# Kernel tuning notes

Measured on AMD Instinct MI355X. Metric: run time of the kernel, lower is better.

Reference implementation:

```python
import jax, jax.numpy as jnp
import numpy as np

EPS = 1e-6
BN_EPS = 1e-5


def point_cells(loc_orig, H, W):
    # map [-1,1] xy coords to nearest cell index on an HxW grid
    loc = jnp.clip(loc_orig, -1.0, 1.0) * 0.5 + 0.5
    cx = jnp.clip(jnp.round(loc[..., 0] * (W - 1)), 0, W - 1).astype(jnp.int32)
    cy = jnp.clip(jnp.round(loc[..., 1] * (H - 1)), 0, H - 1).astype(jnp.int32)
    return cx + cy * W  # (B, N0)


def token2map(x, loc_orig, idx_agg, H, W):
    # scatter token features to an HxW map, averaging per cell
    B, N, C = x.shape
    N0 = loc_orig.shape[1]
    cell = point_cells(loc_orig, H, W)                      # (B, N0)
    feat = jnp.take_along_axis(x, idx_agg[..., None], axis=1)  # (B, N0, C)
    flat = (cell + jnp.arange(B)[:, None] * (H * W)).reshape(-1)
    s = jax.ops.segment_sum(feat.reshape(-1, C), flat, num_segments=B * H * W)
    cnt = jax.ops.segment_sum(jnp.ones((B * N0,), x.dtype), flat, num_segments=B * H * W)
    x_map = s / (cnt[:, None] + EPS)
    return x_map.reshape(B, H, W, C)


def map2token(x_map, N, loc_orig, idx_agg, agg_weight):
    # gather map features at original point locations, aggregate per token
    B, H, W, C = x_map.shape
    cell = point_cells(loc_orig, H, W)
    feat = jnp.take_along_axis(x_map.reshape(B, H * W, C), cell[..., None], axis=1)  # (B, N0, C)
    v = agg_weight.reshape(B, -1, 1)
    tflat = (idx_agg + jnp.arange(B)[:, None] * N).reshape(-1)
    s = jax.ops.segment_sum((feat * v).reshape(-1, C), tflat, num_segments=B * N)
    norm = jax.ops.segment_sum(v.reshape(-1), tflat, num_segments=B * N)
    return (s / (norm[:, None] + EPS)).reshape(B, N, C)


def token_cluster_grid(x, loc_orig, idx_agg, weight, H, W):
    # merge tokens into an (H//2)x(W//2) grid with confidence-weighted averaging
    B, N, C = x.shape
    H2, W2 = H // 2, W // 2
    Ns = H2 * W2
    cell = point_cells(loc_orig, H2, W2)                           # (B, N0) new token per point
    v = jnp.take_along_axis(weight, idx_agg[..., None], axis=1)     # (B, N0, 1)
    feat = jnp.take_along_axis(x, idx_agg[..., None], axis=1)       # (B, N0, C)
    flat = (cell + jnp.arange(B)[:, None] * Ns).reshape(-1)
    s = jax.ops.segment_sum((feat * v).reshape(-1, C), flat, num_segments=B * Ns)
    norm = jax.ops.segment_sum(v.reshape(-1), flat, num_segments=B * Ns) + EPS
    x_down = (s / norm[:, None]).reshape(B, Ns, C)
    weight_t = (v.reshape(-1) / norm[flat]).reshape(B, -1, 1)       # per-point normalized weight
    return x_down, cell, weight_t


def reference(x, loc_orig, idx_agg, agg_weight, conv_w, conv_b, skip_w, bn_gamma, bn_beta, conf_w, conf_b, H, W):
    B, N, C = x.shape
    x_map = token2map(x, loc_orig, idx_agg, H, W)  # (B, H, W, C)
    y = jax.lax.conv_general_dilated(
        x_map, conv_w, window_strides=(2, 2), padding=((1, 1), (1, 1)),
        dimension_numbers=('NHWC', 'HWIO', 'NHWC')) + conv_b  # (B, H/2, W/2, dim_out)
    xt = map2token(y, N, loc_orig, idx_agg, agg_weight) + x @ skip_w  # (B, N, dim_out)
    # BatchNorm over (B, N) per channel (training-mode batch stats)
    mean = jnp.mean(xt, axis=(0, 1))
    var = jnp.var(xt, axis=(0, 1))
    xt = (xt - mean) * jax.lax.rsqrt(var + BN_EPS) * bn_gamma + bn_beta
    conf = xt @ conf_w + conf_b          # (B, N, 1)
    weight = jnp.exp(conf)
    x_down, idx_agg_down, weight_t = token_cluster_grid(xt, loc_orig, idx_agg, weight, H, W)
    agg_weight_down = agg_weight * weight_t
    agg_weight_down = agg_weight_down / jnp.max(agg_weight_down, axis=1, keepdims=True)
    x_down = jax.nn.relu(x_down)
    x_act = jax.nn.relu(xt)
    return x_down, idx_agg_down, agg_weight_down, x_act, conf


def setup_inputs() -> dict:
    key = jax.random.key(0)
    ks = jax.random.split(key, 8)
    B, N, C, Cout, H, W = 64, 4096, 64, 128, 64, 64
    x = jax.random.normal(ks[0], (B, N, C), dtype=jnp.float32)
    loc_orig = jax.random.uniform(ks[1], (B, N, 2), dtype=jnp.float32, minval=-1.0, maxval=1.0)
    idx_agg = jax.random.randint(ks[2], (B, N), 0, N, dtype=jnp.int32)
    agg_weight = jax.random.uniform(ks[3], (B, N, 1), dtype=jnp.float32, minval=0.1, maxval=1.0)
    conv_w = jax.random.normal(ks[4], (3, 3, C, Cout), dtype=jnp.float32) * (1.0 / np.sqrt(9 * C))
    conv_b = jnp.zeros((Cout,), jnp.float32)
    skip_w = jax.random.normal(ks[5], (C, Cout), dtype=jnp.float32) * (1.0 / np.sqrt(C))
    bn_gamma = jnp.ones((Cout,), jnp.float32)
    bn_beta = jnp.zeros((Cout,), jnp.float32)
    conf_w = jax.random.normal(ks[6], (Cout, 1), dtype=jnp.float32) * (1.0 / np.sqrt(Cout))
    conf_b = jnp.zeros((1,), jnp.float32)
    return {"x": x, "loc_orig": loc_orig, "idx_agg": idx_agg, "agg_weight": agg_weight,
            "conv_w": conv_w, "conv_b": conv_b, "skip_w": skip_w,
            "bn_gamma": bn_gamma, "bn_beta": bn_beta, "conf_w": conf_w, "conf_b": conf_b,
            "H": H, "W": W}
```

## Files before the change

### kernel.cpp

```cpp
#include <hip/hip_runtime.h>

#define BB 64
#define NN 4096
#define CCH 64
#define CO 128
#define HH 64
#define WW 64
#define H2 32
#define W2 32
#define EPSF 1e-6f
#define BNEPS 1e-5f

typedef unsigned short ushort_t;
using bf8  = __attribute__((ext_vector_type(8))) short;
using f32x4 = __attribute__((ext_vector_type(4))) float;

__device__ inline ushort_t f2bf(float f) {
  unsigned u = __float_as_uint(f);
  unsigned r = (u + 0x7fffu + ((u >> 16) & 1u)) >> 16;
  return (ushort_t)r;
}
__device__ inline float bflo(unsigned u) { return __uint_as_float(u << 16); }
__device__ inline float bfhi(unsigned u) { return __uint_as_float(u & 0xffff0000u); }

__device__ inline void gload_lds16(const void* src, void* ldsdst) {
  __builtin_amdgcn_global_load_lds((const __attribute__((address_space(1))) void*)src,
                                   (__attribute__((address_space(3))) void*)ldsdst, 16, 0, 0);
}

__device__ inline void cells_from_loc(float lx, float ly, int& c64, int& c32) {
  lx = fminf(fmaxf(lx, -1.f), 1.f) * 0.5f + 0.5f;
  ly = fminf(fmaxf(ly, -1.f), 1.f) * 0.5f + 0.5f;
  int cx = (int)fminf(fmaxf(rintf(lx * (WW - 1)), 0.f), (float)(WW - 1));
  int cy = (int)fminf(fmaxf(rintf(ly * (HH - 1)), 0.f), (float)(HH - 1));
  c64 = cx + cy * WW;
  int cx2 = (int)fminf(fmaxf(rintf(lx * (W2 - 1)), 0.f), (float)(W2 - 1));
  int cy2 = (int)fminf(fmaxf(rintf(ly * (H2 - 1)), 0.f), (float)(H2 - 1));
  c32 = cx2 + cy2 * W2;
}

__global__ __launch_bounds__(256) void k_prep(const float* __restrict__ loc, const int* __restrict__ idxagg,
                                              const float* __restrict__ aw,
                                              float* __restrict__ idx_out,
                                              unsigned* __restrict__ pck64, unsigned* __restrict__ pck32,
                                              unsigned* __restrict__ pckT, float* __restrict__ nrm) {
  int i = blockIdx.x * 256 + threadIdx.x;
  int b = i >> 12;
  int c64, c2;
  cells_from_loc(loc[2 * i], loc[2 * i + 1], c64, c2);
  idx_out[i] = (float)c2;
  atomicAdd(&pck64[(b << 12) + c64], 1u);
  atomicAdd(&pck32[(b << 10) + c2], 1u);
  atomicAdd(&pckT[(b << 12) + idxagg[i]], 1u);
  unsafeAtomicAdd(&nrm[(b << 12) + idxagg[i]], aw[i]);
}

__global__ __launch_bounds__(256) void k_wprep(const float* __restrict__ convw, const float* __restrict__ skipw,
                                               ushort_t* __restrict__ wT, ushort_t* __restrict__ swT) {
  int e = blockIdx.x * 256 + threadIdx.x;
  if (e < 9 * CCH * CO) {
    int co = e & 127, k = e >> 7;
    wT[co * 576 + k] = f2bf(convw[k * CO + co]);
  } else {
    int e2 = e - 9 * CCH * CO;
    int co = e2 & 127, k = e2 >> 7;
    swT[co * 64 + k] = f2bf(skipw[k * CO + co]);
  }
}

__device__ void block_exscan_pack(unsigned* __restrict__ buf, int L) {
  __shared__ int partial[256];
  int tid = threadIdx.x;
  int per = L >> 8;
  int base = tid * per;
  int s = 0;
  for (int i = 0; i < per; i++) s += (int)buf[base + i];
  __syncthreads();
  partial[tid] = s;
  __syncthreads();
  for (int d = 1; d < 256; d <<= 1) {
    int v = (tid >= d) ? partial[tid - d] : 0;
    __syncthreads();
    partial[tid] += v;
    __syncthreads();
  }
  int run = (tid == 0) ? 0 : partial[tid - 1];
  for (int i = 0; i < per; i++) {
    int n = (int)buf[base + i];
    buf[base + i] = ((unsigned)run << 16) | (unsigned)run;
    run += n;
  }
}

__global__ __launch_bounds__(256) void k_scan(unsigned* __restrict__ pck64, unsigned* __restrict__ pckT,
                                              unsigned* __restrict__ pck32) {
  int b = blockIdx.x;
  block_exscan_pack(pck64 + ((size_t)b << 12), 4096);
  block_exscan_pack(pckT + ((size_t)b << 12), 4096);
  block_exscan_pack(pck32 + ((size_t)b << 10), 1024);
}

__global__ __launch_bounds__(256) void k_fill(const float* __restrict__ loc, const int* __restrict__ idxagg,
                                              const float* __restrict__ aw,
                                              unsigned* __restrict__ pck64, unsigned* __restrict__ pckT,
                                              unsigned* __restrict__ pck32,
                                              ushort_t* __restrict__ list64, unsigned* __restrict__ listT,
                                              ushort_t* __restrict__ list32) {
  int i = blockIdx.x * 256 + threadIdx.x;
  int b = i >> 12;
  int c64, c2;
  cells_from_loc(loc[2 * i], loc[2 * i + 1], c64, c2);
  int idx = idxagg[i];
  unsigned pos = atomicAdd(&pck64[(b << 12) + c64], 1u) & 0xffffu;
  list64[(b << 12) + pos] = (ushort_t)idx;
  pos = atomicAdd(&pckT[(b << 12) + idx], 1u) & 0xffffu;
  listT[(b << 12) + pos] = ((unsigned)c2 << 16) | (unsigned)f2bf(aw[i]);
  pos = atomicAdd(&pck32[(b << 10) + c2], 1u) & 0xffffu;
  list32[(b << 12) + pos] = (ushort_t)idx;
}

__global__ __launch_bounds__(256) void k_border(ushort_t* __restrict__ xmb) {
  int t = blockIdx.x * 256 + threadIdx.x;
  int q = t & 15;
  int cell = (t >> 4) % 260;
  int b = t / (260 * 16);
  int r, c;
  if (cell < 66)       { r = 0;  c = cell; }
  else if (cell < 132) { r = 65; c = cell - 66; }
  else if (cell < 196) { r = cell - 132 + 1; c = 0; }
  else                 { r = cell - 196 + 1; c = 65; }
  *(uint2*)&xmb[(((size_t)(b * 66 + r)) * 66 + c) * 64 + q * 4] = make_uint2(0u, 0u);
}

__global__ __launch_bounds__(256) void k_t2m(const float* __restrict__ x,
                                             const unsigned* __restrict__ pck64,
                                             const ushort_t* __restrict__ list64, ushort_t* __restrict__ xmb) {
  int blk = blockIdx.x;
  int sblk = (blk & 7) * 8192 + (blk >> 3);
  int g = sblk * 4 + (threadIdx.x >> 6);
  int lane = threadIdx.x & 63;
  int b = g >> 12, cell = g & 4095;
  unsigned v = pck64[g];
  int o = (int)(v >> 16), n = (int)(v & 0xffffu) - o;
  const ushort_t* lp = list64 + ((size_t)b << 12) + o;
  const float* xb = x + ((size_t)b << 18);
  float s0 = 0.f, s1 = 0.f, s2 = 0.f, s3 = 0.f;
  int i = 0;
  for (; i + 4 <= n; i += 4) {
    int i0 = lp[i], i1 = lp[i + 1], i2 = lp[i + 2], i3 = lp[i + 3];
    s0 += xb[(size_t)i0 * 64 + lane];
    s1 += xb[(size_t)i1 * 64 + lane];
    s2 += xb[(size_t)i2 * 64 + lane];
    s3 += xb[(size_t)i3 * 64 + lane];
  }
  for (; i < n; i++) s0 += xb[(size_t)lp[i] * 64 + lane];
  float avg = (s0 + s1 + s2 + s3) / ((float)n + EPSF);
  int r = cell >> 6, cc = cell & 63;
  xmb[(((size_t)(b * 66 + r + 1)) * 66 + cc + 1) * 64 + lane] = f2bf(avg);
}

__global__ __launch_bounds__(256) void k_conv(const ushort_t* __restrict__ xmb, const ushort_t* __restrict__ wT,
                                              const float* __restrict__ cb, float* __restrict__ y) {
  __shared__ ushort_t A[2][4096];
  const int tid = threadIdx.x;
  const int wave = tid >> 6, lane = tid & 63;
  const int m0 = blockIdx.x * 128;

  f32x4 acc[2][8];
  {
    float bv[8];
#pragma unroll
    for (int nt = 0; nt < 8; nt++) bv[nt] = cb[nt * 16 + (lane & 15)];
#pragma unroll
    for (int mt = 0; mt < 2; mt++)
#pragma unroll
      for (int nt = 0; nt < 8; nt++) {
        f32x4 a; a[0] = bv[nt]; a[1] = bv[nt]; a[2] = bv[nt]; a[3] = bv[nt];
        acc[mt][nt] = a;
      }
  }

  const int srcslot = (((lane & 3) ^ ((lane >> 3) & 3))) * 8;
  int sb[2], soy[2], sox[2];
#pragma unroll
  for (int q = 0; q < 2; q++) {
    int r = wave * 32 + q * 16 + (lane >> 2);
    int s = m0 + r;
    sb[q] = s >> 10; soy[q] = (s >> 5) & 31; sox[q] = s & 31;
  }

  auto stage = [&](int ks, int buf) {
    int kp = ks >> 1, ci0 = (ks & 1) * 32;
    int ky = kp / 3, kx = kp - ky * 3;
#pragma unroll
    for (int q = 0; q < 2; q++) {
      int iy = 2 * soy[q] + ky, ix = 2 * sox[q] + kx;
      const ushort_t* src = xmb + (((size_t)sb[q] * 66 + iy) * 66 + ix) * 64 + ci0 + srcslot;
      gload_lds16(src, &A[buf][(wave * 32 + q * 16) * 32]);
    }
  };

  stage(0, 0);
  const int rdslotx = (lane >> 1) & 3;
  for (int ks = 0; ks < 18; ks++) {
    int buf = ks & 1;
    __syncthreads();
    if (ks < 17) stage(ks + 1, buf ^ 1);
    bf8 a[2];
#pragma unroll
    for (int mt = 0; mt < 2; mt++) {
      int r = wave * 32 + mt * 16 + (lane & 15);
      int slot = (lane >> 4) ^ rdslotx;
      a[mt] = *(const bf8*)&A[buf][r * 32 + slot * 8];
    }
    int k0 = ks * 32 + (lane >> 4) * 8;
#pragma unroll
    for (int nt = 0; nt < 8; nt++) {
      int co = nt * 16 + (lane & 15);
      bf8 bbf = *(const bf8*)&wT[co * 576 + k0];
      acc[0][nt] = __builtin_amdgcn_mfma_f32_16x16x32_bf16(a[0], bbf, acc[0][nt], 0, 0, 0);
      acc[1][nt] = __builtin_amdgcn_mfma_f32_16x16x32_bf16(a[1], bbf, acc[1][nt], 0, 0, 0);
    }
  }
#pragma unroll
  for (int mt = 0; mt < 2; mt++)
#pragma unroll
    for (int nt = 0; nt < 8; nt++) {
      int co = nt * 16 + (lane & 15);
#pragma unroll
      for (int j = 0; j < 4; j++) {
        int srow = m0 + wave * 32 + mt * 16 + (lane >> 4) * 4 + j;
        y[(size_t)srow * 128 + co] = acc[mt][nt][j];
      }
    }
}

__global__ __launch_bounds__(256) void k_xt(const float* __restrict__ x, const ushort_t* __restrict__ swT,
                                            const float* __restrict__ y,
                                            const unsigned* __restrict__ listT, const unsigned* __restrict__ pckT,
                                            const float* __restrict__ nrm,
                                            ushort_t* __restrict__ XTB, float* __restrict__ BNP) {
  __shared__ float xg[64 * 128];
  __shared__ float nrminv[64];
  __shared__ float bnred[256];
  const int tid = threadIdx.x, wave = tid >> 6, lane = tid & 63;
  int blk = blockIdx.x;
  int sblk = (blk & 7) * 512 + (blk >> 3);
  const int t0 = sblk * 64;
  const int b = t0 >> 12, lt0 = t0 & 4095;

#pragma unroll
  for (int q = 0; q < 4; q++) {
    int ch = wave * 4 + q;
    int r = ch * 4 + (lane >> 4);
    int sp = lane & 15;
    const float* src = x + ((size_t)(t0 + r)) * 64 + ((sp ^ (r & 7)) << 2);
    gload_lds16(src, (char*)xg + ch * 1024);
  }
  if (tid < 64) nrminv[tid] = 1.f / (nrm[(b << 12) + lt0 + tid] + EPSF);
  bnred[tid] = 0.f;
  __syncthreads();

  bf8 afr[2];
  {
    int r = wave * 16 + (lane & 15);
#pragma unroll
    for (int ks = 0; ks < 2; ks++) {
      int cs = ks * 4 + (lane >> 4);
      const float4 f0 = *(const float4*)&xg[r * 64 + (((2 * cs) ^ (r & 7)) << 2)];
      const float4 f1 = *(const float4*)&xg[r * 64 + (((2 * cs + 1) ^ (r & 7)) << 2)];
      bf8 v;
      v[0] = (short)f2bf(f0.x); v[1] = (short)f2bf(f0.y);
      v[2] = (short)f2bf(f0.z); v[3] = (short)f2bf(f0.w);
      v[4] = (short)f2bf(f1.x); v[5] = (short)f2bf(f1.y);
      v[6] = (short)f2bf(f1.z); v[7] = (short)f2bf(f1.w);
      afr[ks] = v;
    }
  }

  f32x4 acc[8];
#pragma unroll
  for (int nt = 0; nt < 8; nt++) { f32x4 z; z[0] = 0; z[1] = 0; z[2] = 0; z[3] = 0; acc[nt] = z; }
#pragma unroll
  for (int ks = 0; ks < 2; ks++)
#pragma unroll
    for (int nt = 0; nt < 8; nt++) {
      int co = nt * 16 + (lane & 15);
      bf8 bbf = *(const bf8*)&swT[co * 64 + ks * 32 + (lane >> 4) * 8];
      acc[nt] = __builtin_amdgcn_mfma_f32_16x16x32_bf16(afr[ks], bbf, acc[nt], 0, 0, 0);
    }

  __syncthreads();

#pragma unroll
  for (int rr = 0; rr < 16; rr++) {
    *(float2*)&xg[(wave * 16 + rr) * 128 + ((2 * lane) ^ ((rr & 7) << 4))] = make_float2(0.f, 0.f);
  }

  {
    int gtok = lt0 + wave * 16 + lane;
    int myoff = 0;
    if (lane <= 16) myoff = (gtok >= NN) ? NN : (int)(pckT[(b << 12) + gtok] >> 16);
    int pbeg = __shfl(myoff, 0, 64), pend = __shfl(myoff, 16, 64);
    const unsigned* ltb = listT + ((size_t)b << 12);
    const float* yb = y + ((size_t)b << 17);
    for (int chunk = pbeg; chunk < pend; chunk += 64) {
      int pid = chunk + lane;
      unsigned rec = 0u;
      if (pid < pend) rec = ltb[pid];
      int rr = 0;
#pragma unroll
      for (int j = 1; j <= 16; j++) rr += (pid >= __shfl(myoff, j, 64)) ? 1 : 0;
      int nrec = min(64, pend - chunk);
      int i = 0;
      for (; i + 4 <= nrec; i += 4) {
        float2 yv[4]; float vv[4]; int rw[4];
#pragma unroll
        for (int u = 0; u < 4; u++) {
          unsigned rb = (unsigned)__shfl((int)rec, i + u, 64);
          vv[u] = __uint_as_float(rb << 16);
          rw[u] = __shfl(rr, i + u, 64);
          yv[u] = *(const float2*)&yb[(size_t)(rb >> 16) * 128 + lane * 2];
        }
#pragma unroll
        for (int u = 0; u < 4; u++) {
          float2* p = (float2*)&xg[(wave * 16 + rw[u]) * 128 + ((2 * lane) ^ ((rw[u] & 7) << 4))];
          float2 cv = *p;
          cv.x += yv[u].x * vv[u]; cv.y += yv[u].y * vv[u];
          *p = cv;
        }
      }
      for (; i < nrec; i++) {
        unsigned rb = (unsigned)__shfl((int)rec, i, 64);
        float v = __uint_as_float(rb << 16);
        int rw0 = __shfl(rr, i, 64);
        float2 yv0 = *(const float2*)&yb[(size_t)(rb >> 16) * 128 + lane * 2];
        float2* p = (float2*)&xg[(wave * 16 + rw0) * 128 + ((2 * lane) ^ ((rw0 & 7) << 4))];
        float2 cv = *p;
        cv.x += yv0.x * v; cv.y += yv0.y * v;
        *p = cv;
      }
    }
  }

#pragma unroll
  for (int nt = 0; nt < 8; nt++) {
    int co = nt * 16 + (lane & 15);
    float s = 0.f, q = 0.f;
#pragma unroll
    for (int j = 0; j < 4; j++) {
      int r = wave * 16 + (lane >> 4) * 4 + j;
      float val = acc[nt][j] + xg[r * 128 + (co ^ ((r & 7) << 4))] * nrminv[r];
      acc[nt][j] = val;
      s += val; q += val * val;
    }
    s += __shfl_xor(s, 16, 64); s += __shfl_xor(s, 32, 64);
    q += __shfl_xor(q, 16, 64); q += __shfl_xor(q, 32, 64);
    if (lane < 16) {
      atomicAdd(&bnred[nt * 16 + lane], s);
      atomicAdd(&bnred[128 + nt * 16 + lane], q);
    }
  }
  __syncthreads();

  ushort_t* xto = (ushort_t*)xg;
#pragma unroll
  for (int nt = 0; nt < 8; nt++) {
    int co = nt * 16 + (lane & 15);
#pragma unroll
    for (int j = 0; j < 4; j++) {
      int r = wave * 16 + (lane >> 4) * 4 + j;
      xto[r * 128 + (co ^ ((r & 7) << 4))] = f2bf(acc[nt][j]);
    }
  }
  __syncthreads();
#pragma unroll
  for (int it = 0; it < 4; it++) {
    int q8 = (it * 256 + tid) * 8;
    int r = q8 >> 7, c = q8 & 127;
    uint4 vv = *(const uint4*)&xto[r * 128 + (c ^ ((r & 7) << 4))];
    *(uint4*)&XTB[((size_t)t0) * 128 + q8] = vv;
  }
  unsafeAtomicAdd(&BNP[(blk & 63) * 256 + tid], bnred[tid]);
}

__global__ void k_bnfin(const float* __restrict__ BNP, const float* __restrict__ gamma,
                        const float* __restrict__ beta, float* __restrict__ ss) {
  int c = threadIdx.x;
  float s = 0.f, q = 0.f;
#pragma unroll 4
  for (int k = 0; k < 64; k++) {
    s += BNP[k * 256 + c];
    q += BNP[k * 256 + 128 + c];
  }
  float n = (float)(BB * NN);
  float mean = s / n;
  float var = q / n - mean * mean;
  float sc = gamma[c] * rsqrtf(var + BNEPS);
  ss[c] = sc;
  ss[128 + c] = beta[c] - mean * sc;
}

__global__ __launch_bounds__(256) void k_conf(const ushort_t* __restrict__ XTB, const float* __restrict__ ss,
                                              const float* __restrict__ confw, const float* __restrict__ confb,
                                              float* __restrict__ conf_out, float* __restrict__ wgt,
                                              float* __restrict__ xa) {
  int gid = blockIdx.x * 256 + threadIdx.x;
  int p = gid >> 6, lane = gid & 63;
  unsigned pw = *(const unsigned*)&XTB[(size_t)p * 128 + 2 * lane];
  const float2 sc = *(const float2*)&ss[2 * lane];
  const float2 sh = *(const float2*)&ss[128 + 2 * lane];
  float v0 = bflo(pw) * sc.x + sh.x;
  float v1 = bfhi(pw) * sc.y + sh.y;
  float2 xo; xo.x = fmaxf(v0, 0.f); xo.y = fmaxf(v1, 0.f);
  *(float2*)&xa[(size_t)p * 128 + 2 * lane] = xo;
  const float2 cw = *(const float2*)&confw[2 * lane];
  float s = v0 * cw.x + v1 * cw.y;
#pragma unroll
  for (int off = 32; off; off >>= 1) s += __shfl_down(s, off, 64);
  if (lane == 0) {
    float cf = s + confb[0];
    conf_out[p] = cf;
    wgt[p] = __expf(cf);
  }
}

__global__ __launch_bounds__(256) void k_cluster(const ushort_t* __restrict__ XTB, const float* __restrict__ ss,
                                                 const float* __restrict__ wgt,
                                                 const unsigned* __restrict__ pck32,
                                                 const ushort_t* __restrict__ list32,
                                                 float* __restrict__ xd, float* __restrict__ cnrm) {
  int blk = blockIdx.x;
  int sblk = (blk & 7) * 2048 + (blk >> 3);
  int wid = sblk * 4 + (threadIdx.x >> 6);
  int lane = threadIdx.x & 63;
  int b = wid >> 10;
  unsigned v = pck32[wid];
  int o = (int)(v >> 16), n = (int)(v & 0xffffu) - o;
  const ushort_t* lp = list32 + ((size_t)b << 12) + o;
  const float* wb = wgt + ((size_t)b << 12);
  const ushort_t* xtb = XTB + (((size_t)b) << 19);
  const float2 sc = *(const float2*)&ss[2 * lane];
  const float2 sh = *(const float2*)&ss[128 + 2 * lane];
  float s0 = 0.f, s1 = 0.f, sv = 0.f;
  int i = 0;
  for (; i + 2 <= n; i += 2) {
    int i0 = lp[i], i1 = lp[i + 1];
    float v0 = wb[i0], v1 = wb[i1];
    unsigned p0 = *(const unsigned*)&xtb[(size_t)i0 * 128 + 2 * lane];
    unsigned p1 = *(const unsigned*)&xtb[(size_t)i1 * 128 + 2 * lane];
    s0 += (bflo(p0) * sc.x + sh.x) * v0 + (bflo(p1) * sc.x + sh.x) * v1;
    s1 += (bfhi(p0) * sc.y + sh.y) * v0 + (bfhi(p1) * sc.y + sh.y) * v1;
    sv += v0 + v1;
  }
  if (i < n) {
    int i0 = lp[i];
    float v0 = wb[i0];
    unsigned p0 = *(const unsigned*)&xtb[(size_t)i0 * 128 + 2 * lane];
    s0 += (bflo(p0) * sc.x + sh.x) * v0;
    s1 += (bfhi(p0) * sc.y + sh.y) * v0;
    sv += v0;
  }
  float inv = 1.f / (sv + EPSF);
  float2 o2; o2.x = fmaxf(s0 * inv, 0.f); o2.y = fmaxf(s1 * inv, 0.f);
  *(float2*)&xd[(size_t)wid * 128 + 2 * lane] = o2;
  if (lane == 0) cnrm[wid] = sv;
}

__global__ __launch_bounds__(256) void k_awd(const float* __restrict__ loc, const float* __restrict__ wgt,
                                             const float* __restrict__ aw, const int* __restrict__ idxagg,
                                             const float* __restrict__ cnrm,
                                             float* __restrict__ awd, int* __restrict__ maxb) {
  int p = blockIdx.x * 256 + threadIdx.x;
  int b = p >> 12;
  int c64, c2;
  cells_from_loc(loc[2 * p], loc[2 * p + 1], c64, c2);
  float v = wgt[(b << 12) + idxagg[p]];
  float wt = v / (cnrm[(b << 10) + c2] + EPSF);
  float a = aw[p] * wt;
  awd[p] = a;
  float m = a;
#pragma unroll
  for (int off = 32; off; off >>= 1) m = fmaxf(m, __shfl_down(m, off, 64));
  if ((threadIdx.x & 63) == 0) atomicMax(&maxb[b], __float_as_int(m));
}

__global__ __launch_bounds__(256) void k_awdnorm(float* __restrict__ awd, const int* __restrict__ maxb) {
  int p = blockIdx.x * 256 + threadIdx.x;
  int b = p >> 12;
  awd[p] = awd[p] / __int_as_float(maxb[b]);
}

extern "C" void kernel_launch(void* const* d_in, const int* in_sizes, int n_in,
                              void* d_out, int out_size, void* d_ws, size_t ws_size,
                              hipStream_t stream) {
  (void)in_sizes; (void)n_in; (void)out_size;
  const float* x      = (const float*)d_in[0];
  const float* loc    = (const float*)d_in[1];
  const int*   idxagg = (const int*)  d_in[2];
  const float* aw     = (const float*)d_in[3];
  const float* convw  = (const float*)d_in[4];
  const float* convb  = (const float*)d_in[5];
  const float* skipw  = (const float*)d_in[6];
  const float* gamma  = (const float*)d_in[7];
  const float* beta   = (const float*)d_in[8];
  const float* confw  = (const float*)d_in[9];
  const float* confb  = (const float*)d_in[10];

  char* ws = (char*)d_ws;
  ushort_t* XTB   = (ushort_t*)(ws + 0);
  float*    Y     = (float*)  (ws + 67108864);
  ushort_t* XMB   = (ushort_t*)(ws + 100663296);
  float*    WGT   = (float*)  (ws + 100663296);
  float*    CNRM  = (float*)  (ws + 101711872);
  float*    BNP   = (float*)  (ws + 101974016);
  float*    SS    = (float*)  (ws + 102039552);
  int*      MAXB  = (int*)    (ws + 102040576);
  ushort_t* WT    = (ushort_t*)(ws + 136347648);
  ushort_t* SWT   = (ushort_t*)(ws + 136495104);
  float*    NRM   = (float*)  (ws + 136511488);
  unsigned* PCK64 = (unsigned*)(ws + 137560064);
  ushort_t* LIST64= (ushort_t*)(ws + 138608640);
  unsigned* PCKT  = (unsigned*)(ws + 139132928);
  unsigned* LISTT = (unsigned*)(ws + 140181504);
  unsigned* PCK32 = (unsigned*)(ws + 141230080);
  ushort_t* LIST32= (ushort_t*)(ws + 141492224);
  if (ws_size < 142016512) return;

  float* out    = (float*)d_out;
  float* O_XD   = out;
  float* O_IDX  = out + 8388608;
  float* O_AWD  = out + 8650752;
  float* XA     = out + 8912896;
  float* O_CONF = out + 42467328;

  hipMemsetAsync(PCK64, 0, 1048576, stream);
  hipMemsetAsync(PCKT, 0, 1048576, stream);
  hipMemsetAsync(PCK32, 0, 262144, stream);
  hipMemsetAsync(NRM, 0, 1048576, stream);

  k_prep   <<<1024,  256, 0, stream>>>(loc, idxagg, aw, O_IDX, PCK64, PCK32, PCKT, NRM);
  k_wprep  <<<320,   256, 0, stream>>>(convw, skipw, WT, SWT);
  k_scan   <<<64,    256, 0, stream>>>(PCK64, PCKT, PCK32);
  k_fill   <<<1024,  256, 0, stream>>>(loc, idxagg, aw, PCK64, PCKT, PCK32, LIST64, LISTT, LIST32);
  k_border <<<1040,  256, 0, stream>>>(XMB);
  k_t2m    <<<65536, 256, 0, stream>>>(x, PCK64, LIST64, XMB);
  k_conv   <<<512,   256, 0, stream>>>(XMB, WT, convb, Y);
  hipMemsetAsync(BNP, 0, 65536, stream);
  hipMemsetAsync(MAXB, 0, 256, stream);
  k_xt     <<<4096,  256, 0, stream>>>(x, SWT, Y, LISTT, PCKT, NRM, XTB, BNP);
  k_bnfin  <<<1,     128, 0, stream>>>(BNP, gamma, beta, SS);
  k_conf   <<<65536, 256, 0, stream>>>(XTB, SS, confw, confb, O_CONF, WGT, XA);
  k_cluster<<<16384, 256, 0, stream>>>(XTB, SS, WGT, PCK32, LIST32, O_XD, CNRM);
  k_awd    <<<1024,  256, 0, stream>>>(loc, WGT, aw, idxagg, CNRM, O_AWD, MAXB);
  k_awdnorm<<<1024,  256, 0, stream>>>(O_AWD, MAXB);
}
```

Measured before the change: 389.2 us.

## Fuse awd into cluster kernel, store conv output as bf16, consolidate memsets

Several changes land together. The conv output Y is stored as bf16 instead of fp32, which halves its write and gather traffic in k_xt at some precision cost. The k_awd kernel is folded into k_cluster: list32 now carries the point index, so the weights and the per-batch max are computed there. k_conf is vectorized to four channels per thread, k_scan is split across three times as many blocks, and the workspace is repacked so one memset covers all the zeroed buffers.

```diff
diff --git a/kernel.cpp b/kernel.cpp
--- a/kernel.cpp
+++ b/kernel.cpp
@@ -94,10 +94,10 @@
 
 __global__ __launch_bounds__(256) void k_scan(unsigned* __restrict__ pck64, unsigned* __restrict__ pckT,
                                               unsigned* __restrict__ pck32) {
-  int b = blockIdx.x;
-  block_exscan_pack(pck64 + ((size_t)b << 12), 4096);
-  block_exscan_pack(pckT + ((size_t)b << 12), 4096);
-  block_exscan_pack(pck32 + ((size_t)b << 10), 1024);
+  int b = blockIdx.x / 3, kind = blockIdx.x - 3 * (blockIdx.x / 3);
+  if (kind == 0)      block_exscan_pack(pck64 + ((size_t)b << 12), 4096);
+  else if (kind == 1) block_exscan_pack(pckT + ((size_t)b << 12), 4096);
+  else                block_exscan_pack(pck32 + ((size_t)b << 10), 1024);
 }
 
 __global__ __launch_bounds__(256) void k_fill(const float* __restrict__ loc, const int* __restrict__ idxagg,
@@ -105,9 +105,9 @@
                                               unsigned* __restrict__ pck64, unsigned* __restrict__ pckT,
                                               unsigned* __restrict__ pck32,
                                               ushort_t* __restrict__ list64, unsigned* __restrict__ listT,
-                                              ushort_t* __restrict__ list32) {
+                                              unsigned* __restrict__ list32) {
   int i = blockIdx.x * 256 + threadIdx.x;
-  int b = i >> 12;
+  int b = i >> 12, p = i & 4095;
   int c64, c2;
   cells_from_loc(loc[2 * i], loc[2 * i + 1], c64, c2);
   int idx = idxagg[i];
@@ -116,7 +116,7 @@
   pos = atomicAdd(&pckT[(b << 12) + idx], 1u) & 0xffffu;
   listT[(b << 12) + pos] = ((unsigned)c2 << 16) | (unsigned)f2bf(aw[i]);
   pos = atomicAdd(&pck32[(b << 10) + c2], 1u) & 0xffffu;
-  list32[(b << 12) + pos] = (ushort_t)idx;
+  list32[(b << 12) + pos] = ((unsigned)idx << 16) | (unsigned)p;
 }
 
 __global__ __launch_bounds__(256) void k_border(ushort_t* __restrict__ xmb) {
@@ -160,7 +160,7 @@
 }
 
 __global__ __launch_bounds__(256) void k_conv(const ushort_t* __restrict__ xmb, const ushort_t* __restrict__ wT,
-                                              const float* __restrict__ cb, float* __restrict__ y) {
+                                              const float* __restrict__ cb, ushort_t* __restrict__ y) {
   __shared__ ushort_t A[2][4096];
   const int tid = threadIdx.x;
   const int wave = tid >> 6, lane = tid & 63;
@@ -230,13 +230,13 @@
 #pragma unroll
       for (int j = 0; j < 4; j++) {
         int srow = m0 + wave * 32 + mt * 16 + (lane >> 4) * 4 + j;
-        y[(size_t)srow * 128 + co] = acc[mt][nt][j];
+        y[(size_t)srow * 128 + co] = f2bf(acc[mt][nt][j]);
       }
     }
 }
 
 __global__ __launch_bounds__(256) void k_xt(const float* __restrict__ x, const ushort_t* __restrict__ swT,
-                                            const float* __restrict__ y,
+                                            const ushort_t* __restrict__ y,
                                             const unsigned* __restrict__ listT, const unsigned* __restrict__ pckT,
                                             const float* __restrict__ nrm,
                                             ushort_t* __restrict__ XTB, float* __restrict__ BNP) {
@@ -303,7 +303,7 @@
     if (lane <= 16) myoff = (gtok >= NN) ? NN : (int)(pckT[(b << 12) + gtok] >> 16);
     int pbeg = __shfl(myoff, 0, 64), pend = __shfl(myoff, 16, 64);
     const unsigned* ltb = listT + ((size_t)b << 12);
-    const float* yb = y + ((size_t)b << 17);
+    const ushort_t* yb = y + ((size_t)b << 17);
     for (int chunk = pbeg; chunk < pend; chunk += 64) {
       int pid = chunk + lane;
       unsigned rec = 0u;
@@ -314,19 +314,19 @@
       int nrec = min(64, pend - chunk);
       int i = 0;
       for (; i + 4 <= nrec; i += 4) {
-        float2 yv[4]; float vv[4]; int rw[4];
+        unsigned yu[4]; float vv[4]; int rw[4];
 #pragma unroll
         for (int u = 0; u < 4; u++) {
           unsigned rb = (unsigned)__shfl((int)rec, i + u, 64);
           vv[u] = __uint_as_float(rb << 16);
           rw[u] = __shfl(rr, i + u, 64);
-          yv[u] = *(const float2*)&yb[(size_t)(rb >> 16) * 128 + lane * 2];
+          yu[u] = *(const unsigned*)&yb[(size_t)(rb >> 16) * 128 + lane * 2];
         }
 #pragma unroll
         for (int u = 0; u < 4; u++) {
           float2* p = (float2*)&xg[(wave * 16 + rw[u]) * 128 + ((2 * lane) ^ ((rw[u] & 7) << 4))];
           float2 cv = *p;
-          cv.x += yv[u].x * vv[u]; cv.y += yv[u].y * vv[u];
+          cv.x += bflo(yu[u]) * vv[u]; cv.y += bfhi(yu[u]) * vv[u];
           *p = cv;
         }
       }
@@ -334,10 +334,10 @@
         unsigned rb = (unsigned)__shfl((int)rec, i, 64);
         float v = __uint_as_float(rb << 16);
         int rw0 = __shfl(rr, i, 64);
-        float2 yv0 = *(const float2*)&yb[(size_t)(rb >> 16) * 128 + lane * 2];
+        unsigned yu0 = *(const unsigned*)&yb[(size_t)(rb >> 16) * 128 + lane * 2];
         float2* p = (float2*)&xg[(wave * 16 + rw0) * 128 + ((2 * lane) ^ ((rw0 & 7) << 4))];
         float2 cv = *p;
-        cv.x += yv0.x * v; cv.y += yv0.y * v;
+        cv.x += bflo(yu0) * v; cv.y += bfhi(yu0) * v;
         *p = cv;
       }
     }
@@ -406,19 +406,24 @@
                                               float* __restrict__ conf_out, float* __restrict__ wgt,
                                               float* __restrict__ xa) {
   int gid = blockIdx.x * 256 + threadIdx.x;
-  int p = gid >> 6, lane = gid & 63;
-  unsigned pw = *(const unsigned*)&XTB[(size_t)p * 128 + 2 * lane];
-  const float2 sc = *(const float2*)&ss[2 * lane];
-  const float2 sh = *(const float2*)&ss[128 + 2 * lane];
-  float v0 = bflo(pw) * sc.x + sh.x;
-  float v1 = bfhi(pw) * sc.y + sh.y;
-  float2 xo; xo.x = fmaxf(v0, 0.f); xo.y = fmaxf(v1, 0.f);
-  *(float2*)&xa[(size_t)p * 128 + 2 * lane] = xo;
-  const float2 cw = *(const float2*)&confw[2 * lane];
-  float s = v0 * cw.x + v1 * cw.y;
-#pragma unroll
-  for (int off = 32; off; off >>= 1) s += __shfl_down(s, off, 64);
-  if (lane == 0) {
+  int p = gid >> 5, l32 = gid & 31;
+  int c0 = l32 * 4;
+  const uint2 pw = *(const uint2*)&XTB[(size_t)p * 128 + c0];
+  const float4 sc = *(const float4*)&ss[c0];
+  const float4 sh = *(const float4*)&ss[128 + c0];
+  float v0 = bflo(pw.x) * sc.x + sh.x;
+  float v1 = bfhi(pw.x) * sc.y + sh.y;
+  float v2 = bflo(pw.y) * sc.z + sh.z;
+  float v3 = bfhi(pw.y) * sc.w + sh.w;
+  float4 xo;
+  xo.x = fmaxf(v0, 0.f); xo.y = fmaxf(v1, 0.f);
+  xo.z = fmaxf(v2, 0.f); xo.w = fmaxf(v3, 0.f);
+  *(float4*)&xa[(size_t)p * 128 + c0] = xo;
+  const float4 cw = *(const float4*)&confw[c0];
+  float s = v0 * cw.x + v1 * cw.y + v2 * cw.z + v3 * cw.w;
+#pragma unroll
+  for (int off = 16; off; off >>= 1) s += __shfl_down(s, off, 32);
+  if (l32 == 0) {
     float cf = s + confb[0];
     conf_out[p] = cf;
     wgt[p] = __expf(cf);
@@ -426,26 +431,30 @@
 }
 
 __global__ __launch_bounds__(256) void k_cluster(const ushort_t* __restrict__ XTB, const float* __restrict__ ss,
-                                                 const float* __restrict__ wgt,
+                                                 const float* __restrict__ wgt, const float* __restrict__ aw,
                                                  const unsigned* __restrict__ pck32,
-                                                 const ushort_t* __restrict__ list32,
-                                                 float* __restrict__ xd, float* __restrict__ cnrm) {
+                                                 const unsigned* __restrict__ list32,
+                                                 float* __restrict__ xd, float* __restrict__ awd,
+                                                 int* __restrict__ maxb) {
+  __shared__ float smax[4];
   int blk = blockIdx.x;
   int sblk = (blk & 7) * 2048 + (blk >> 3);
-  int wid = sblk * 4 + (threadIdx.x >> 6);
-  int lane = threadIdx.x & 63;
+  int wave = threadIdx.x >> 6, lane = threadIdx.x & 63;
+  int wid = sblk * 4 + wave;
   int b = wid >> 10;
   unsigned v = pck32[wid];
   int o = (int)(v >> 16), n = (int)(v & 0xffffu) - o;
-  const ushort_t* lp = list32 + ((size_t)b << 12) + o;
+  const unsigned* lp = list32 + ((size_t)b << 12) + o;
   const float* wb = wgt + ((size_t)b << 12);
+  const float* awb = aw + ((size_t)b << 12);
   const ushort_t* xtb = XTB + (((size_t)b) << 19);
   const float2 sc = *(const float2*)&ss[2 * lane];
   const float2 sh = *(const float2*)&ss[128 + 2 * lane];
   float s0 = 0.f, s1 = 0.f, sv = 0.f;
   int i = 0;
   for (; i + 2 <= n; i += 2) {
-    int i0 = lp[i], i1 = lp[i + 1];
+    unsigned r0 = lp[i], r1 = lp[i + 1];
+    int i0 = r0 >> 16, i1 = r1 >> 16;
     float v0 = wb[i0], v1 = wb[i1];
     unsigned p0 = *(const unsigned*)&xtb[(size_t)i0 * 128 + 2 * lane];
     unsigned p1 = *(const unsigned*)&xtb[(size_t)i1 * 128 + 2 * lane];
@@ -454,7 +463,8 @@
     sv += v0 + v1;
   }
   if (i < n) {
-    int i0 = lp[i];
+    unsigned r0 = lp[i];
+    int i0 = r0 >> 16;
     float v0 = wb[i0];
     unsigned p0 = *(const unsigned*)&xtb[(size_t)i0 * 128 + 2 * lane];
     s0 += (bflo(p0) * sc.x + sh.x) * v0;
@@ -464,25 +474,23 @@
   float inv = 1.f / (sv + EPSF);
   float2 o2; o2.x = fmaxf(s0 * inv, 0.f); o2.y = fmaxf(s1 * inv, 0.f);
   *(float2*)&xd[(size_t)wid * 128 + 2 * lane] = o2;
-  if (lane == 0) cnrm[wid] = sv;
-}
-
-__global__ __launch_bounds__(256) void k_awd(const float* __restrict__ loc, const float* __restrict__ wgt,
-                                             const float* __restrict__ aw, const int* __restrict__ idxagg,
-                                             const float* __restrict__ cnrm,
-                                             float* __restrict__ awd, int* __restrict__ maxb) {
-  int p = blockIdx.x * 256 + threadIdx.x;
-  int b = p >> 12;
-  int c64, c2;
-  cells_from_loc(loc[2 * p], loc[2 * p + 1], c64, c2);
-  float v = wgt[(b << 12) + idxagg[p]];
-  float wt = v / (cnrm[(b << 10) + c2] + EPSF);
-  float a = aw[p] * wt;
-  awd[p] = a;
-  float m = a;
-#pragma unroll
-  for (int off = 32; off; off >>= 1) m = fmaxf(m, __shfl_down(m, off, 64));
-  if ((threadIdx.x & 63) == 0) atomicMax(&maxb[b], __float_as_int(m));
+
+  float mymax = 0.f;
+  for (int k = lane; k < n; k += 64) {
+    unsigned rec = lp[k];
+    int idx = rec >> 16, pp = rec & 0xffffu;
+    float a = awb[pp] * wb[idx] * inv;
+    awd[(b << 12) + pp] = a;
+    mymax = fmaxf(mymax, a);
+  }
+#pragma unroll
+  for (int off = 32; off; off >>= 1) mymax = fmaxf(mymax, __shfl_down(mymax, off, 64));
+  if (lane == 0) smax[wave] = mymax;
+  __syncthreads();
+  if (threadIdx.x == 0) {
+    float m = fmaxf(fmaxf(smax[0], smax[1]), fmaxf(smax[2], smax[3]));
+    atomicMax(&maxb[b], __float_as_int(m));
+  }
 }
 
 __global__ __launch_bounds__(256) void k_awdnorm(float* __restrict__ awd, const int* __restrict__ maxb) {
@@ -509,23 +517,22 @@
 
   char* ws = (char*)d_ws;
   ushort_t* XTB   = (ushort_t*)(ws + 0);
-  float*    Y     = (float*)  (ws + 67108864);
-  ushort_t* XMB   = (ushort_t*)(ws + 100663296);
-  float*    WGT   = (float*)  (ws + 100663296);
-  float*    CNRM  = (float*)  (ws + 101711872);
-  float*    BNP   = (float*)  (ws + 101974016);
-  float*    SS    = (float*)  (ws + 102039552);
-  int*      MAXB  = (int*)    (ws + 102040576);
-  ushort_t* WT    = (ushort_t*)(ws + 136347648);
-  ushort_t* SWT   = (ushort_t*)(ws + 136495104);
-  float*    NRM   = (float*)  (ws + 136511488);
-  unsigned* PCK64 = (unsigned*)(ws + 137560064);
-  ushort_t* LIST64= (ushort_t*)(ws + 138608640);
-  unsigned* PCKT  = (unsigned*)(ws + 139132928);
-  unsigned* LISTT = (unsigned*)(ws + 140181504);
-  unsigned* PCK32 = (unsigned*)(ws + 141230080);
-  ushort_t* LIST32= (ushort_t*)(ws + 141492224);
-  if (ws_size < 142016512) return;
+  ushort_t* XMB   = (ushort_t*)(ws + 0);
+  ushort_t* Y     = (ushort_t*)(ws + 67108864);
+  ushort_t* WT    = (ushort_t*)(ws + 83886080);
+  ushort_t* SWT   = (ushort_t*)(ws + 84033536);
+  unsigned* PCK64 = (unsigned*)(ws + 84049920);
+  unsigned* PCKT  = (unsigned*)(ws + 85098496);
+  unsigned* PCK32 = (unsigned*)(ws + 86147072);
+  float*    NRM   = (float*)  (ws + 86409216);
+  float*    BNP   = (float*)  (ws + 87457792);
+  int*      MAXB  = (int*)    (ws + 87523328);
+  ushort_t* LIST64= (ushort_t*)(ws + 87524352);
+  unsigned* LISTT = (unsigned*)(ws + 88048640);
+  unsigned* LIST32= (unsigned*)(ws + 89097216);
+  float*    WGT   = (float*)  (ws + 90145792);
+  float*    SS    = (float*)  (ws + 91194368);
+  if (ws_size < 91195392) return;
 
   float* out    = (float*)d_out;
   float* O_XD   = out;
@@ -534,24 +541,18 @@
   float* XA     = out + 8912896;
   float* O_CONF = out + 42467328;
 
-  hipMemsetAsync(PCK64, 0, 1048576, stream);
-  hipMemsetAsync(PCKT, 0, 1048576, stream);
-  hipMemsetAsync(PCK32, 0, 262144, stream);
-  hipMemsetAsync(NRM, 0, 1048576, stream);
+  hipMemsetAsync(PCK64, 0, 3474432, stream);
 
   k_prep   <<<1024,  256, 0, stream>>>(loc, idxagg, aw, O_IDX, PCK64, PCK32, PCKT, NRM);
   k_wprep  <<<320,   256, 0, stream>>>(convw, skipw, WT, SWT);
-  k_scan   <<<64,    256, 0, stream>>>(PCK64, PCKT, PCK32);
+  k_scan   <<<192,   256, 0, stream>>>(PCK64, PCKT, PCK32);
   k_fill   <<<1024,  256, 0, stream>>>(loc, idxagg, aw, PCK64, PCKT, PCK32, LIST64, LISTT, LIST32);
   k_border <<<1040,  256, 0, stream>>>(XMB);
   k_t2m    <<<65536, 256, 0, stream>>>(x, PCK64, LIST64, XMB);
   k_conv   <<<512,   256, 0, stream>>>(XMB, WT, convb, Y);
-  hipMemsetAsync(BNP, 0, 65536, stream);
-  hipMemsetAsync(MAXB, 0, 256, stream);
   k_xt     <<<4096,  256, 0, stream>>>(x, SWT, Y, LISTT, PCKT, NRM, XTB, BNP);
   k_bnfin  <<<1,     128, 0, stream>>>(BNP, gamma, beta, SS);
-  k_conf   <<<65536, 256, 0, stream>>>(XTB, SS, confw, confb, O_CONF, WGT, XA);
-  k_cluster<<<16384, 256, 0, stream>>>(XTB, SS, WGT, PCK32, LIST32, O_XD, CNRM);
-  k_awd    <<<1024,  256, 0, stream>>>(loc, WGT, aw, idxagg, CNRM, O_AWD, MAXB);
+  k_conf   <<<32768, 256, 0, stream>>>(XTB, SS, confw, confb, O_CONF, WGT, XA);
+  k_cluster<<<16384, 256, 0, stream>>>(XTB, SS, WGT, aw, PCK32, LIST32, O_XD, O_AWD, MAXB);
   k_awdnorm<<<1024,  256, 0, stream>>>(O_AWD, MAXB);
 }
```

Result: slower. 407.2 us (+4.6%).
